# Kernel optimization log

Hardware: AMD Instinct MI355X
Metric: run time of the kernel (lower is better)

The kernel has to match this reference:

```python
import jax, jax.numpy as jnp
import numpy as np
from jax import lax

NUM_HEADS = 8
HEAD_DIM = 32
DIM = NUM_HEADS * HEAD_DIM  # 256
SR = 2
B, H, W = 4, 64, 64


def setup_inputs() -> dict:
    key = jax.random.key(0)
    ks = jax.random.split(key, 6)
    x = jax.random.normal(ks[0], (B, DIM, H, W), dtype=jnp.float32)
    # query: 1x1 conv without bias -> plain [out,in] matrix
    Wq = jax.random.normal(ks[1], (DIM, DIM), dtype=jnp.float32) * (1.0 / np.sqrt(DIM))
    # key/value: sr x sr conv, stride sr, no bias (OIHW)
    Wk = jax.random.normal(ks[2], (DIM, DIM, SR, SR), dtype=jnp.float32) * (1.0 / np.sqrt(DIM * SR * SR))
    Wv = jax.random.normal(ks[3], (DIM, DIM, SR, SR), dtype=jnp.float32) * (1.0 / np.sqrt(DIM * SR * SR))
    rel_h = jax.random.normal(ks[4], (1, NUM_HEADS, HEAD_DIM, 1, H // SR), dtype=jnp.float32)
    rel_w = jax.random.normal(ks[5], (1, NUM_HEADS, HEAD_DIM, W // SR, 1), dtype=jnp.float32)
    return {"x": x, "Wq": Wq, "Wk": Wk, "Wv": Wv, "rel_h": rel_h, "rel_w": rel_w}


def reference(x, Wq, Wk, Wv, rel_h, rel_w):
    b, c, h, w = x.shape
    nh, hd = NUM_HEADS, HEAD_DIM
    scale = hd ** (-0.5)
    dn = ('NCHW', 'OIHW', 'NCHW')

    # q: 1x1 conv == channel matmul; [B, C, H*W] -> [B, nh, hd, Nq]
    q = jnp.einsum('oc,bchw->bohw', Wq, x).reshape(b, nh, hd, h * w)
    # k, v: sr x sr conv, stride sr -> [B, nh, hd, Nkv]
    k = lax.conv_general_dilated(x, Wk, window_strides=(SR, SR), padding='VALID',
                                 dimension_numbers=dn).reshape(b, nh, hd, -1)
    v = lax.conv_general_dilated(x, Wv, window_strides=(SR, SR), padding='VALID',
                                 dimension_numbers=dn).reshape(b, nh, hd, -1)

    # attn scores: q^T k -> [B, nh, Nq, Nkv]
    attn = jnp.einsum('bhdn,bhdm->bhnm', q, k)
    # relative positional bias: (rel_h + rel_w) broadcast -> [nh, hd, Nkv]
    pos = (rel_h + rel_w).reshape(nh, hd, -1)
    attn = attn + jnp.einsum('bhdn,hdm->bhnm', q, pos)
    attn = jax.nn.softmax(attn * scale, axis=-1)

    # out = v @ attn^T -> [B, nh, hd, Nq] -> [B, C, H, W]
    out = jnp.einsum('bhdm,bhnm->bhdn', v, attn).reshape(b, c, h, w)
    return out
```

## Files before the change

### kernel.cpp

```cpp
#include <hip/hip_runtime.h>
#include <math.h>


typedef __bf16 bf16;
typedef __attribute__((ext_vector_type(4))) __bf16 bf16x4;
typedef __attribute__((ext_vector_type(8))) __bf16 bf16x8;
typedef __attribute__((ext_vector_type(4))) float f32x4;
typedef __attribute__((ext_vector_type(2))) __fp16 fp16x2_raw;
typedef __attribute__((ext_vector_type(4))) _Float16 f16x4;

#define MFMA16 __builtin_amdgcn_mfma_f32_16x16x32_bf16
#define MFMA16H __builtin_amdgcn_mfma_f32_16x16x16f16

#define QSCALE 0.25503486f
#define SOFTMAX_SHIFT 10.0f

__global__ void k_prep_w(const float* __restrict__ Wq, const float* __restrict__ Wk,
                         const float* __restrict__ Wv,
                         bf16* __restrict__ Wq_bf, bf16* __restrict__ Wkv_bf) {
    int tid = blockIdx.x * 256 + threadIdx.x;
    int c = tid >> 8, i = tid & 255;
    const float* Wsrc = (c < 256) ? Wk : Wv;
    int cs = c & 255;
    f32x4 w4 = ((const f32x4*)Wsrc)[cs * 256 + i];
#pragma unroll
    for (int tap = 0; tap < 4; tap++)
        Wkv_bf[c * 1024 + tap * 256 + i] = (bf16)w4[tap];
    if (tid < 16384) {
        f32x4 q4 = ((const f32x4*)Wq)[tid];
        bf16x4 o;
#pragma unroll
        for (int e = 0; e < 4; e++) o[e] = (bf16)(q4[e] * QSCALE);
        *(bf16x4*)(Wq_bf + tid * 4) = o;
    }
}

__global__ void k_xT(const float* __restrict__ x, bf16* __restrict__ xT) {
    int b = blockIdx.z, c0 = blockIdx.y * 64, n0 = blockIdx.x * 64;
    __shared__ float tile[64][65];
    int t = threadIdx.x;
    const float* xp = x + (size_t)(b * 256 + c0) * 4096 + n0;
#pragma unroll
    for (int k2 = 0; k2 < 16; k2++) {
        int flat = k2 * 256 + t;
        int row = flat >> 6, col = flat & 63;
        tile[row][col] = xp[(size_t)row * 4096 + col];
    }
    __syncthreads();
    bf16* op = xT + (size_t)(b * 4096 + n0) * 256 + c0;
#pragma unroll
    for (int k2 = 0; k2 < 16; k2++) {
        int flat = k2 * 256 + t;
        int row = flat >> 6, col = flat & 63;
        op[(size_t)row * 256 + col] = (bf16)tile[col][row];
    }
}

__launch_bounds__(256)
__global__ void k_gemm_kv(const bf16* __restrict__ xT, const bf16* __restrict__ Wkv_bf,
                          const float* __restrict__ rel_h, const float* __restrict__ rel_w,
                          bf16* __restrict__ kpos_t, _Float16* __restrict__ v_td) {
    int b = blockIdx.z;
    int bx = blockIdx.x;
    int m0 = bx * 32;
    int c0w = blockIdx.y * 64 + (threadIdx.x >> 6) * 16;
    int t = threadIdx.x, l = t & 63;
    int lr = l & 15, lg = l >> 4;
    __shared__ __align__(16) bf16 Ps[2][32 * 264];
    const bf16* xb = xT + (size_t)b * 4096 * 256;
    int srow = t >> 3;
    int scu0 = (t & 7) * 4;
    uint4 pre[4];
#define LOAD_CHUNK(tap)                                                        \
    {                                                                          \
        int dy = (tap) >> 1, dx = (tap) & 1;                                   \
        const bf16* src = xb + (size_t)((2 * bx + dy) * 64 + 2 * srow + dx) * 256; \
        _Pragma("unroll")                                                      \
        for (int j = 0; j < 4; j++)                                            \
            pre[j] = *(const uint4*)(src + (scu0 + j) * 8);                    \
    }
#define WRITE_CHUNK(buf)                                                       \
    {                                                                          \
        bf16* dst = Ps[buf] + srow * 264 + scu0 * 8;                           \
        _Pragma("unroll")                                                      \
        for (int j = 0; j < 4; j++) *(uint4*)(dst + j * 8) = pre[j];           \
    }
    LOAD_CHUNK(0)
    WRITE_CHUNK(0)
    const bf16* Gkb = Wkv_bf + (size_t)(c0w + lr) * 1024 + lg * 8;
    const bf16* Gvb = Gkb + 256 * 1024;
    f32x4 accK[2] = {}, accV[2] = {};
    for (int ch = 0; ch < 4; ch++) {
        if (ch < 3) LOAD_CHUNK(ch + 1)
        __syncthreads();
        const bf16* P = Ps[ch & 1];
#pragma unroll
        for (int kk = 0; kk < 8; kk++) {
            bf16x8 pa0 = *(const bf16x8*)(P + lr * 264 + kk * 32 + lg * 8);
            bf16x8 pa1 = *(const bf16x8*)(P + (16 + lr) * 264 + kk * 32 + lg * 8);
            bf16x8 gk = *(const bf16x8*)(Gkb + ch * 256 + kk * 32);
            bf16x8 gv = *(const bf16x8*)(Gvb + ch * 256 + kk * 32);
            accK[0] = MFMA16(pa0, gk, accK[0], 0, 0, 0);
            accK[1] = MFMA16(pa1, gk, accK[1], 0, 0, 0);
            accV[0] = MFMA16(gv, pa0, accV[0], 0, 0, 0);
            accV[1] = MFMA16(gv, pa1, accV[1], 0, 0, 0);
        }
        if (ch < 3) {
            __syncthreads();
            WRITE_CHUNK((ch + 1) & 1)
        }
    }
    {
        int cc = c0w + lr;
        float rw = rel_w[cc * 32 + bx];
#pragma unroll
        for (int i = 0; i < 2; i++)
#pragma unroll
            for (int r = 0; r < 4; r++) {
                int ml = i * 16 + lg * 4 + r;
                float val = accK[i][r] + rw + rel_h[cc * 32 + ml];
                kpos_t[((size_t)(b * 8 + (cc >> 5)) * 1024 + m0 + ml) * 32 + (cc & 31)] = (bf16)val;
            }
    }
#pragma unroll
    for (int j = 0; j < 2; j++) {
        int m = m0 + j * 16 + lr;
#pragma unroll
        for (int r = 0; r < 4; r++) {
            int cc = c0w + lg * 4 + r;
            v_td[((size_t)(b * 8 + (cc >> 5)) * 32 + (cc & 31)) * 1024 + m] = (_Float16)accV[j][r];
        }
    }
#undef LOAD_CHUNK
#undef WRITE_CHUNK
}

__launch_bounds__(256, 4)
__global__ void k_attn(const bf16* __restrict__ xT, const bf16* __restrict__ Wq_bf,
                       const bf16* __restrict__ kpos_t, const _Float16* __restrict__ v_td,
                       float* __restrict__ out) {
    int b = blockIdx.z, h = blockIdx.y;
    int t = threadIdx.x;
    int w = t >> 6, l = t & 63;
    int n0 = blockIdx.x * 128 + w * 32;
    int lr = l & 15, lg = l >> 4;
    const size_t bh = (size_t)(b * 8 + h);
    __shared__ __align__(16) bf16 Ks[256 * 32];
    __shared__ __align__(16) _Float16 Vs[32][264];
    const bf16* Kb = kpos_t + bh * 1024 * 32;
    const _Float16* Vb = v_td + bh * 32 * 1024;
    uint4 kpre[4], vpre[4];
#define LOAD_PASS(pass)                                                        \
    {                                                                          \
        const uint4* ksrc = (const uint4*)(Kb + (size_t)(pass) * 256 * 32);    \
        _Pragma("unroll")                                                      \
        for (int j = 0; j < 4; j++) kpre[j] = ksrc[t + j * 256];               \
        _Pragma("unroll")                                                      \
        for (int j = 0; j < 4; j++) {                                          \
            int u = t + j * 256;                                               \
            vpre[j] = *(const uint4*)(Vb + (size_t)(u >> 5) * 1024 +           \
                                      (pass) * 256 + (u & 31) * 8);            \
        }                                                                      \
    }
#define WRITE_PASS()                                                           \
    {                                                                          \
        uint4* kdst = (uint4*)Ks;                                              \
        _Pragma("unroll")                                                      \
        for (int j = 0; j < 4; j++) kdst[t + j * 256] = kpre[j];               \
        _Pragma("unroll")                                                      \
        for (int j = 0; j < 4; j++) {                                          \
            int u = t + j * 256;                                               \
            *(uint4*)(&Vs[u >> 5][(u & 31) * 8]) = vpre[j];                    \
        }                                                                      \
    }
    LOAD_PASS(0)
    bf16* Qs = Ks + w * 1280;
    {
        const bf16* Aw = Wq_bf + (size_t)(h * 32 + lr) * 256 + lg * 8;
        const bf16* Bx = xT + (size_t)(b * 4096 + n0 + lr) * 256 + lg * 8;
        f32x4 aq[2][2] = {};
#pragma unroll
        for (int kk = 0; kk < 8; kk++) {
            bf16x8 a0 = *(const bf16x8*)(Aw + kk * 32);
            bf16x8 a1 = *(const bf16x8*)(Aw + 16 * 256 + kk * 32);
            bf16x8 b0 = *(const bf16x8*)(Bx + kk * 32);
            bf16x8 b1 = *(const bf16x8*)(Bx + 16 * 256 + kk * 32);
            aq[0][0] = MFMA16(a0, b0, aq[0][0], 0, 0, 0);
            aq[0][1] = MFMA16(a0, b1, aq[0][1], 0, 0, 0);
            aq[1][0] = MFMA16(a1, b0, aq[1][0], 0, 0, 0);
            aq[1][1] = MFMA16(a1, b1, aq[1][1], 0, 0, 0);
        }
#pragma unroll
        for (int i = 0; i < 2; i++)
#pragma unroll
            for (int j = 0; j < 2; j++) {
                bf16x4 pk;
#pragma unroll
                for (int r = 0; r < 4; r++) pk[r] = (bf16)aq[i][j][r];
                *(bf16x4*)(Qs + (j * 16 + lr) * 40 + i * 16 + lg * 4) = pk;
            }
    }
    bf16x8 bq0, bq1;
    {
        bf16x4 a0 = *(const bf16x4*)(Qs + lr * 40 + lg * 8);
        bf16x4 a1 = *(const bf16x4*)(Qs + lr * 40 + lg * 8 + 4);
        bf16x4 b0 = *(const bf16x4*)(Qs + (16 + lr) * 40 + lg * 8);
        bf16x4 b1 = *(const bf16x4*)(Qs + (16 + lr) * 40 + lg * 8 + 4);
#pragma unroll
        for (int e = 0; e < 4; e++) {
            bq0[e] = a0[e]; bq0[4 + e] = a1[e];
            bq1[e] = b0[e]; bq1[4 + e] = b1[e];
        }
    }
    __syncthreads();
    WRITE_PASS()
    f32x4 accO[2][2] = {};
    f32x4 accS0 = {}, accS1 = {};
    const f16x4 onesv = {(_Float16)1.f, (_Float16)1.f, (_Float16)1.f, (_Float16)1.f};
    const f32x4 zs = {-SOFTMAX_SHIFT, -SOFTMAX_SHIFT, -SOFTMAX_SHIFT, -SOFTMAX_SHIFT};
    for (int pass = 0; pass < 4; pass++) {
        if (pass < 3) LOAD_PASS(pass + 1)
        __syncthreads();
#pragma unroll 4
        for (int tt = 0; tt < 16; tt++) {
            bf16x8 ak = *(const bf16x8*)(Ks + (tt * 16 + lr) * 32 + lg * 8);
            f32x4 s0 = MFMA16(ak, bq0, zs, 0, 0, 0);
            f32x4 s1 = MFMA16(ak, bq1, zs, 0, 0, 0);
            f16x4 p0, p1;
            {
                fp16x2_raw c01 = __builtin_amdgcn_cvt_pkrtz(
                    __builtin_amdgcn_exp2f(fminf(s0[0], 16.f)),
                    __builtin_amdgcn_exp2f(fminf(s0[1], 16.f)));
                fp16x2_raw c23 = __builtin_amdgcn_cvt_pkrtz(
                    __builtin_amdgcn_exp2f(fminf(s0[2], 16.f)),
                    __builtin_amdgcn_exp2f(fminf(s0[3], 16.f)));
                p0[0] = c01[0]; p0[1] = c01[1]; p0[2] = c23[0]; p0[3] = c23[1];
                fp16x2_raw d01 = __builtin_amdgcn_cvt_pkrtz(
                    __builtin_amdgcn_exp2f(fminf(s1[0], 16.f)),
                    __builtin_amdgcn_exp2f(fminf(s1[1], 16.f)));
                fp16x2_raw d23 = __builtin_amdgcn_cvt_pkrtz(
                    __builtin_amdgcn_exp2f(fminf(s1[2], 16.f)),
                    __builtin_amdgcn_exp2f(fminf(s1[3], 16.f)));
                p1[0] = d01[0]; p1[1] = d01[1]; p1[2] = d23[0]; p1[3] = d23[1];
            }
            f16x4 v0 = *(const f16x4*)(&Vs[lr][tt * 16 + lg * 4]);
            f16x4 v1 = *(const f16x4*)(&Vs[16 + lr][tt * 16 + lg * 4]);
            accO[0][0] = MFMA16H(p0, v0, accO[0][0], 0, 0, 0);
            accO[0][1] = MFMA16H(p0, v1, accO[0][1], 0, 0, 0);
            accS0      = MFMA16H(p0, onesv, accS0, 0, 0, 0);
            accO[1][0] = MFMA16H(p1, v0, accO[1][0], 0, 0, 0);
            accO[1][1] = MFMA16H(p1, v1, accO[1][1], 0, 0, 0);
            accS1      = MFMA16H(p1, onesv, accS1, 0, 0, 0);
        }
        if (pass < 3) {
            __syncthreads();
            WRITE_PASS()
        }
    }
#undef LOAD_PASS
#undef WRITE_PASS
    float inv0[4], inv1[4];
#pragma unroll
    for (int r = 0; r < 4; r++) {
        inv0[r] = 1.0f / accS0[r];
        inv1[r] = 1.0f / accS1[r];
    }
#pragma unroll
    for (int dt = 0; dt < 2; dt++) {
        int c = h * 32 + dt * 16 + lr;
        float* op0 = out + (size_t)(b * 256 + c) * 4096 + n0 + lg * 4;
        float* op1 = op0 + 16;
        f32x4 o0, o1;
#pragma unroll
        for (int r = 0; r < 4; r++) {
            o0[r] = accO[0][dt][r] * inv0[r];
            o1[r] = accO[1][dt][r] * inv1[r];
        }
        *(f32x4*)op0 = o0;
        *(f32x4*)op1 = o1;
    }
}

extern "C" void kernel_launch(void* const* d_in, const int* in_sizes, int n_in,
                              void* d_out, int out_size, void* d_ws, size_t ws_size,
                              hipStream_t stream) {
    const float* x    = (const float*)d_in[0];
    const float* Wq   = (const float*)d_in[1];
    const float* Wk   = (const float*)d_in[2];
    const float* Wv   = (const float*)d_in[3];
    const float* relh = (const float*)d_in[4];
    const float* relw = (const float*)d_in[5];
    float* out = (float*)d_out;
    char* ws = (char*)d_ws;

    bf16*      xT     = (bf16*)(ws);
    bf16*      kposT  = (bf16*)(ws + (8u << 20));
    _Float16*  v_td   = (_Float16*)(ws + (10u << 20));
    bf16*      Wq_bf  = (bf16*)(ws + (12u << 20));
    bf16*      Wkv_bf = (bf16*)(ws + (12u << 20) + (256u << 10));

    k_prep_w <<<512,            256, 0, stream>>>(Wq, Wk, Wv, Wq_bf, Wkv_bf);
    k_xT     <<<dim3(64, 4, 4), 256, 0, stream>>>(x, xT);
    k_gemm_kv<<<dim3(32, 4, 4), 256, 0, stream>>>(xT, Wkv_bf, relh, relw, kposT, v_td);
    k_attn   <<<dim3(32, 8, 4), 256, 0, stream>>>(xT, Wq_bf, kposT, v_td, out);
}
```

Before: 176.3 us.

## Swizzle K tile in shared memory and drop register prefetch of K/V passes

The K tile is now written into shared memory with a rotated 16-byte chunk layout, and the matching read offset avoids bank conflicts on the bf16x8 K fragment loads. The register-staged prefetch of the next K/V pass is removed, so each pass loads global data straight into shared memory and then synchronises. The launch-bounds occupancy hint is also dropped. This frees the prefetch registers and cuts LDS bank conflicts, but global-load latency is no longer overlapped with the MFMA loop of the previous pass.

```diff
diff --git a/kernel.cpp b/kernel.cpp
--- a/kernel.cpp
+++ b/kernel.cpp
@@ -135,7 +135,7 @@
 #undef WRITE_CHUNK
 }
 
-__launch_bounds__(256, 4)
+__launch_bounds__(256)
 __global__ void k_attn(const bf16* __restrict__ xT, const bf16* __restrict__ Wq_bf,
                        const bf16* __restrict__ kpos_t, const _Float16* __restrict__ v_td,
                        float* __restrict__ out) {
@@ -149,31 +149,6 @@
     __shared__ __align__(16) _Float16 Vs[32][264];
     const bf16* Kb = kpos_t + bh * 1024 * 32;
     const _Float16* Vb = v_td + bh * 32 * 1024;
-    uint4 kpre[4], vpre[4];
-#define LOAD_PASS(pass)                                                        \
-    {                                                                          \
-        const uint4* ksrc = (const uint4*)(Kb + (size_t)(pass) * 256 * 32);    \
-        _Pragma("unroll")                                                      \
-        for (int j = 0; j < 4; j++) kpre[j] = ksrc[t + j * 256];               \
-        _Pragma("unroll")                                                      \
-        for (int j = 0; j < 4; j++) {                                          \
-            int u = t + j * 256;                                               \
-            vpre[j] = *(const uint4*)(Vb + (size_t)(u >> 5) * 1024 +           \
-                                      (pass) * 256 + (u & 31) * 8);            \
-        }                                                                      \
-    }
-#define WRITE_PASS()                                                           \
-    {                                                                          \
-        uint4* kdst = (uint4*)Ks;                                              \
-        _Pragma("unroll")                                                      \
-        for (int j = 0; j < 4; j++) kdst[t + j * 256] = kpre[j];               \
-        _Pragma("unroll")                                                      \
-        for (int j = 0; j < 4; j++) {                                          \
-            int u = t + j * 256;                                               \
-            *(uint4*)(&Vs[u >> 5][(u & 31) * 8]) = vpre[j];                    \
-        }                                                                      \
-    }
-    LOAD_PASS(0)
     bf16* Qs = Ks + w * 1280;
     {
         const bf16* Aw = Wq_bf + (size_t)(h * 32 + lr) * 256 + lg * 8;
@@ -213,17 +188,30 @@
         }
     }
     __syncthreads();
-    WRITE_PASS()
     f32x4 accO[2][2] = {};
     f32x4 accS0 = {}, accS1 = {};
     const f16x4 onesv = {(_Float16)1.f, (_Float16)1.f, (_Float16)1.f, (_Float16)1.f};
     const f32x4 zs = {-SOFTMAX_SHIFT, -SOFTMAX_SHIFT, -SOFTMAX_SHIFT, -SOFTMAX_SHIFT};
+    const int koff = (((lr >> 1) + lg) & 3) * 8;
     for (int pass = 0; pass < 4; pass++) {
-        if (pass < 3) LOAD_PASS(pass + 1)
+        const uint4* ksrc = (const uint4*)(Kb + (size_t)pass * 256 * 32);
+#pragma unroll
+        for (int j = 0; j < 4; j++) {
+            int u = t + j * 256;
+            int m = u >> 2;
+            int phys = ((m >> 1) + (u & 3)) & 3;
+            *(uint4*)(Ks + m * 32 + phys * 8) = ksrc[u];
+        }
+#pragma unroll
+        for (int j = 0; j < 4; j++) {
+            int u = t + j * 256;
+            *(uint4*)(&Vs[u >> 5][(u & 31) * 8]) =
+                *(const uint4*)(Vb + (size_t)(u >> 5) * 1024 + pass * 256 + (u & 31) * 8);
+        }
         __syncthreads();
 #pragma unroll 4
         for (int tt = 0; tt < 16; tt++) {
-            bf16x8 ak = *(const bf16x8*)(Ks + (tt * 16 + lr) * 32 + lg * 8);
+            bf16x8 ak = *(const bf16x8*)(Ks + (tt * 16 + lr) * 32 + koff);
             f32x4 s0 = MFMA16(ak, bq0, zs, 0, 0, 0);
             f32x4 s1 = MFMA16(ak, bq1, zs, 0, 0, 0);
             f16x4 p0, p1;
@@ -252,13 +240,8 @@
             accO[1][1] = MFMA16H(p1, v1, accO[1][1], 0, 0, 0);
             accS1      = MFMA16H(p1, onesv, accS1, 0, 0, 0);
         }
-        if (pass < 3) {
-            __syncthreads();
-            WRITE_PASS()
-        }
-    }
-#undef LOAD_PASS
-#undef WRITE_PASS
+        if (pass < 3) __syncthreads();
+    }
     float inv0[4], inv1[4];
 #pragma unroll
     for (int r = 0; r < 4; r++) {
```

Result: faster. 155.7 us (-11.7%).
